# Kernel optimization log

Hardware: AMD Instinct MI355X
Metric: run time of the kernel (lower is better)

## Reference

```python
import jax, jax.numpy as jnp
import numpy as np

N_E = 1024
E_DIM = 64
BETA = 0.25


def setup_inputs() -> dict:
    key = jax.random.key(0)
    k1, k2 = jax.random.split(key)
    z = jax.random.normal(k1, (16, E_DIM, 64, 64), dtype=jnp.float32)
    # embedding initialized uniform(-1/n_e, 1/n_e) as in the torch module
    emb = jax.random.uniform(k2, (N_E, E_DIM), dtype=jnp.float32,
                             minval=-1.0 / N_E, maxval=1.0 / N_E)
    return {"z": z, "emb": emb}


def reference(z, emb):
    n_e, e_dim = emb.shape
    # NCHW -> NHWC, flatten to tokens
    zp = jnp.transpose(z, (0, 2, 3, 1))            # [B,H,W,C]
    zf = zp.reshape(-1, e_dim)                      # [N,C]
    # squared distances ||zf||^2 + ||e||^2 - 2 zf e^T  -> [N, n_e]
    d = (jnp.sum(zf * zf, axis=1, keepdims=True)
         + jnp.sum(emb * emb, axis=1)
         - 2.0 * jnp.matmul(zf, emb.T))
    idx = jnp.argmin(d, axis=1)                     # [N]
    # one-hot @ emb is exactly a gather
    z_q = emb[idx].reshape(zp.shape)                # [B,H,W,C]
    loss = (jnp.mean((jax.lax.stop_gradient(z_q) - zp) ** 2)
            + BETA * jnp.mean((z_q - jax.lax.stop_gradient(zp)) ** 2))
    # straight-through estimator
    z_q = zp + jax.lax.stop_gradient(z_q - zp)
    # perplexity from codeword usage histogram
    counts = jax.ops.segment_sum(jnp.ones_like(idx, dtype=zf.dtype), idx,
                                 num_segments=n_e)
    e_mean = counts / zf.shape[0]
    perplexity = jnp.exp(-jnp.sum(e_mean * jnp.log(e_mean + 1e-10)))
    min_encoding_indices = idx.reshape(z.shape[0], -1).astype(jnp.int32)
    z_q = jnp.transpose(z_q, (0, 3, 1, 2))          # back to NCHW
    return z_q, loss, perplexity, min_encoding_indices
```

## Files before the change

kernel.cpp:

```cpp
#include <hip/hip_runtime.h>

#define TOKS 65536
#define ED 64
#define NE 1024
#define CH_STRIDE 4096
#define B_STRIDE 262144

typedef __bf16 bf16x8 __attribute__((ext_vector_type(8)));
typedef float f32x16 __attribute__((ext_vector_type(16)));
typedef unsigned short ushort_t;
typedef unsigned int uint_t;


__device__ __forceinline__ ushort_t f2bf(float x) {
    uint_t u = __float_as_uint(x);
    uint_t r = u + 0x7FFFu + ((u >> 16) & 1u);
    return (ushort_t)(r >> 16);
}

__global__ __launch_bounds__(256) void vq_prep_e(const float* __restrict__ emb,
                                                 ushort_t* __restrict__ efrag,
                                                 float* __restrict__ enorm,
                                                 int* __restrict__ hist) {
    const int tid = threadIdx.x;
    const int w = tid >> 6, lane = tid & 63;
    const int j = blockIdx.x * 4 + w;

    const float e = emb[j * 64 + lane];
    const float sq = __fmul_rn(e, e);
    float acc = sq;
    acc = __fadd_rn(acc, __shfl_down(sq, 8, 64));
    acc = __fadd_rn(acc, __shfl_down(sq, 16, 64));
    acc = __fadd_rn(acc, __shfl_down(sq, 24, 64));
    acc = __fadd_rn(acc, __shfl_down(sq, 32, 64));
    acc = __fadd_rn(acc, __shfl_down(sq, 40, 64));
    acc = __fadd_rn(acc, __shfl_down(sq, 48, 64));
    acc = __fadd_rn(acc, __shfl_down(sq, 56, 64));
    float x = __fadd_rn(acc, __shfl_down(acc, 1, 64));
    float y = __fadd_rn(x, __shfl_down(x, 2, 64));
    float zn = __fadd_rn(y, __shfl_down(y, 4, 64));
    if (lane == 0) enorm[j] = zn;

    const ushort_t h = f2bf(-2.0f * e);
    const int ct = j >> 5, m = j & 31;
    const int ks = lane >> 4, kh = (lane >> 3) & 1, i = lane & 7;
    efrag[(size_t)((ct * 4 + ks) * 512) + (m + 32 * kh) * 8 + i] = h;

    if (blockIdx.x < 4) hist[blockIdx.x * 256 + tid] = 0;
}

__global__ __launch_bounds__(256, 4) void vq_main(
    const float* __restrict__ z,
    const ushort_t* __restrict__ efrag,
    const float* __restrict__ enorm,
    const float* __restrict__ emb,
    float* __restrict__ zq,
    float* __restrict__ out_idx,
    int* __restrict__ hist,
    double* __restrict__ lossPart) {
    __shared__ float z_s[32][68];
    __shared__ uint_t skey[4][32][2];
    __shared__ unsigned long long s_res[32];
    __shared__ double wsum[4];

    const int tid = threadIdx.x;
    const int w = tid >> 6, lane = tid & 63;
    const int t0 = blockIdx.x * 32;
    const int b = t0 >> 12, hw0 = t0 & 4095;
    const float* zbase = z + (size_t)b * B_STRIDE + hw0;

    {
        const int c = tid >> 2, u0 = (tid & 3) * 8;
        const float* src = zbase + (size_t)c * CH_STRIDE + u0;
        float4 f0 = *(const float4*)(src);
        float4 f1 = *(const float4*)(src + 4);
        z_s[u0 + 0][c] = f0.x; z_s[u0 + 1][c] = f0.y;
        z_s[u0 + 2][c] = f0.z; z_s[u0 + 3][c] = f0.w;
        z_s[u0 + 4][c] = f1.x; z_s[u0 + 5][c] = f1.y;
        z_s[u0 + 6][c] = f1.z; z_s[u0 + 7][c] = f1.w;
    }
    if (tid < 32) s_res[tid] = 0xFFFFFFFFFFFFFFFFull;
    __syncthreads();

    const int n = lane & 31, kh = lane >> 5;

    bf16x8 zb[4];
    #pragma unroll
    for (int ks = 0; ks < 4; ++ks) {
        float4 a0 = *(const float4*)&z_s[n][ks * 16 + kh * 8];
        float4 a1 = *(const float4*)&z_s[n][ks * 16 + kh * 8 + 4];
        const float av[8] = {a0.x, a0.y, a0.z, a0.w, a1.x, a1.y, a1.z, a1.w};
        #pragma unroll
        for (int i = 0; i < 8; ++i) {
            union { ushort_t u; __bf16 bh; } cv;
            cv.u = f2bf(av[i]);
            zb[ks][i] = cv.bh;
        }
    }

    uint_t k0 = 0xFFFFFFFFu, k1 = 0xFFFFFFFFu;
    const bf16x8* eg = (const bf16x8*)efrag;
    const int rot = blockIdx.x & 7;

    int gct = w * 8 + rot;
    bf16x8 ah0 = eg[(size_t)(gct * 4 + 0) * 64 + lane];
    bf16x8 ah1 = eg[(size_t)(gct * 4 + 1) * 64 + lane];
    bf16x8 ah2 = eg[(size_t)(gct * 4 + 2) * 64 + lane];
    bf16x8 ah3 = eg[(size_t)(gct * 4 + 3) * 64 + lane];

    for (int ct = 0; ct < 8; ++ct) {
        const int gnext = w * 8 + ((ct + 1 + rot) & 7);
        bf16x8 nx0, nx1, nx2, nx3;
        if (ct < 7) {
            nx0 = eg[(size_t)(gnext * 4 + 0) * 64 + lane];
            nx1 = eg[(size_t)(gnext * 4 + 1) * 64 + lane];
            nx2 = eg[(size_t)(gnext * 4 + 2) * 64 + lane];
            nx3 = eg[(size_t)(gnext * 4 + 3) * 64 + lane];
        }
        const int jb = gct * 32 + 4 * kh;

        f32x16 acc;
        #pragma unroll
        for (int r = 0; r < 16; ++r) acc[r] = 0.25f;
        acc = __builtin_amdgcn_mfma_f32_32x32x16_bf16(ah0, zb[0], acc, 0, 0, 0);
        acc = __builtin_amdgcn_mfma_f32_32x32x16_bf16(ah1, zb[1], acc, 0, 0, 0);
        acc = __builtin_amdgcn_mfma_f32_32x32x16_bf16(ah2, zb[2], acc, 0, 0, 0);
        acc = __builtin_amdgcn_mfma_f32_32x32x16_bf16(ah3, zb[3], acc, 0, 0, 0);

        #pragma unroll
        for (int r = 0; r < 16; ++r) {
            uint_t key = (__float_as_uint(acc[r]) & 0xFFFFFC00u)
                         | (uint_t)(jb + (r & 3) + 8 * (r >> 2));
            uint_t mx = max(k0, key);
            k1 = min(k1, mx);
            k0 = min(k0, key);
        }
        ah0 = nx0; ah1 = nx1; ah2 = nx2; ah3 = nx3;
        gct = gnext;
    }

    {
        uint_t p0 = (uint_t)__shfl_xor((int)k0, 32, 64);
        uint_t p1 = (uint_t)__shfl_xor((int)k1, 32, 64);
        uint_t o0 = min(k0, p0);
        uint_t o1 = min(max(k0, p0), min(k1, p1));
        if (kh == 0) { skey[w][n][0] = o0; skey[w][n][1] = o1; }
    }
    __syncthreads();

    const int tok = tid >> 3, p = tid & 7;
    const uint_t ck = skey[p >> 1][tok][p & 1];
    uint_t kmin = ck;
    kmin = min(kmin, (uint_t)__shfl_xor((int)kmin, 1, 64));
    kmin = min(kmin, (uint_t)__shfl_xor((int)kmin, 2, 64));
    kmin = min(kmin, (uint_t)__shfl_xor((int)kmin, 4, 64));
    const float thr = __uint_as_float(kmin & 0xFFFFFC00u) + 4.0e-4f;

    float zn;
    {
        float a = z_s[tok][p];
        float racc = __fmul_rn(a, a);
        #pragma unroll
        for (int i = 1; i < 8; ++i) {
            float av = z_s[tok][p + 8 * i];
            racc = __fadd_rn(racc, __fmul_rn(av, av));
        }
        float x1 = __fadd_rn(racc, __shfl_xor(racc, 1, 64));
        float y1 = __fadd_rn(x1, __shfl_xor(x1, 2, 64));
        zn = __fadd_rn(y1, __shfl_xor(y1, 4, 64));
    }

    if (__uint_as_float(ck & 0xFFFFFC00u) <= thr) {
        const int j = (int)(ck & 1023u);
        const float* e = emb + (size_t)j * 64;
        float a0 = 0.f;
        #pragma unroll
        for (int k4 = 0; k4 < 16; ++k4) {
            float4 z4 = *(const float4*)&z_s[tok][k4 * 4];
            float4 e4 = *(const float4*)(e + k4 * 4);
            a0 = __fmaf_rn(z4.x, e4.x, a0);
            a0 = __fmaf_rn(z4.y, e4.y, a0);
            a0 = __fmaf_rn(z4.z, e4.z, a0);
            a0 = __fmaf_rn(z4.w, e4.w, a0);
        }
        float d = __fsub_rn(__fadd_rn(zn, enorm[j]), 2.0f * a0);
        unsigned long long key =
            ((unsigned long long)__float_as_uint(d) << 10)
            | (unsigned long long)j;
        atomicMin(&s_res[tok], key);
    }
    __syncthreads();

    const int bj = (int)(s_res[tok] & 1023u);
    if (p == 0) {
        out_idx[t0 + tok] = (float)bj;
        atomicAdd(&hist[bj], 1);
    }
    double ls = 0.0;
    {
        const float* e = emb + (size_t)bj * 64 + p * 8;
        float4 e0 = *(const float4*)(e);
        float4 e1 = *(const float4*)(e + 4);
        float4 zv0 = *(const float4*)&z_s[tok][p * 8];
        float4 zv1 = *(const float4*)&z_s[tok][p * 8 + 4];
        float df;
        df = e0.x - zv0.x; ls += (double)(df * df);
        df = e0.y - zv0.y; ls += (double)(df * df);
        df = e0.z - zv0.z; ls += (double)(df * df);
        df = e0.w - zv0.w; ls += (double)(df * df);
        df = e1.x - zv1.x; ls += (double)(df * df);
        df = e1.y - zv1.y; ls += (double)(df * df);
        df = e1.z - zv1.z; ls += (double)(df * df);
        df = e1.w - zv1.w; ls += (double)(df * df);
        *(float4*)&z_s[tok][p * 8] = e0;
        *(float4*)&z_s[tok][p * 8 + 4] = e1;
    }
    #pragma unroll
    for (int off = 32; off > 0; off >>= 1) ls += __shfl_down(ls, off, 64);
    if (lane == 0) wsum[w] = ls;
    __syncthreads();
    if (tid == 0)
        lossPart[blockIdx.x] = wsum[0] + wsum[1] + wsum[2] + wsum[3];

    {
        const int c = tid >> 2, u0 = (tid & 3) * 8;
        float4 f0, f1;
        f0.x = z_s[u0 + 0][c]; f0.y = z_s[u0 + 1][c];
        f0.z = z_s[u0 + 2][c]; f0.w = z_s[u0 + 3][c];
        f1.x = z_s[u0 + 4][c]; f1.y = z_s[u0 + 5][c];
        f1.z = z_s[u0 + 6][c]; f1.w = z_s[u0 + 7][c];
        float* dst = zq + (size_t)b * B_STRIDE + (size_t)c * CH_STRIDE + hw0 + u0;
        *(float4*)(dst) = f0;
        *(float4*)(dst + 4) = f1;
    }
}

__global__ __launch_bounds__(256) void vq_final(const int* __restrict__ hist,
                                                const double* __restrict__ lossPart,
                                                float* __restrict__ outs) {
    __shared__ double red[256];
    __shared__ double red2[256];
    double acc = 0.0;
    for (int j = threadIdx.x; j < NE; j += 256) {
        double em = (double)hist[j] * (1.0 / 65536.0);
        acc += em * log(em + 1e-10);
    }
    double lsum = 0.0;
    for (int j = threadIdx.x; j < 2048; j += 256) lsum += lossPart[j];
    red[threadIdx.x] = acc;
    red2[threadIdx.x] = lsum;
    __syncthreads();
    for (int s = 128; s > 0; s >>= 1) {
        if (threadIdx.x < s) {
            red[threadIdx.x] += red[threadIdx.x + s];
            red2[threadIdx.x] += red2[threadIdx.x + s];
        }
        __syncthreads();
    }
    if (threadIdx.x == 0) {
        outs[0] = (float)(1.25 * red2[0] * (1.0 / 4194304.0));
        outs[1] = (float)exp(-red[0]);
    }
}

extern "C" void kernel_launch(void* const* d_in, const int* in_sizes, int n_in,
                              void* d_out, int out_size, void* d_ws, size_t ws_size,
                              hipStream_t stream) {
    const float* z = (const float*)d_in[0];
    const float* emb = (const float*)d_in[1];
    float* out = (float*)d_out;

    char* ws = (char*)d_ws;
    ushort_t* efrag = (ushort_t*)ws;
    float* enorm = (float*)(ws + 131072);
    int* hist = (int*)(ws + 135168);
    double* lossPart = (double*)(ws + 143360);

    float* zq = out;
    float* scalars = out + 4194304;
    float* out_idx = out + 4194306;

    vq_prep_e<<<256, 256, 0, stream>>>(emb, efrag, enorm, hist);
    vq_main<<<2048, 256, 0, stream>>>(z, efrag, enorm, emb, zq, out_idx,
                                      hist, lossPart);
    vq_final<<<1, 256, 0, stream>>>(hist, lossPart, scalars);
}
```

Baseline: 45.26 us.

## Replace top-2 key tracking with min-threshold pass and selective MFMA recompute

The first pass over codebook tiles now keeps only a per-tile float minimum instead of packing index bits into keys and tracking the top two. A second pass recomputes the bf16 MFMA only for tiles whose minimum falls within a threshold of the global minimum, and rescores every candidate within that threshold in exact fp32. This removes the per-element key packing and top-2 logic and makes candidate selection more robust. The cost is repeated efrag loads and MFMAs for qualifying tiles, divergent fp32 dot products, and the loss of the rotation-based prefetch pipelining.

```diff
diff --git a/kernel.cpp b/kernel.cpp
--- a/kernel.cpp
+++ b/kernel.cpp
@@ -59,7 +59,8 @@
     int* __restrict__ hist,
     double* __restrict__ lossPart) {
     __shared__ float z_s[32][68];
-    __shared__ uint_t skey[4][32][2];
+    __shared__ float sminf[4][32];
+    __shared__ float s_zn[32];
     __shared__ unsigned long long s_res[32];
     __shared__ double wsum[4];
 
@@ -98,27 +99,16 @@
         }
     }
 
-    uint_t k0 = 0xFFFFFFFFu, k1 = 0xFFFFFFFFu;
     const bf16x8* eg = (const bf16x8*)efrag;
-    const int rot = blockIdx.x & 7;
-
-    int gct = w * 8 + rot;
-    bf16x8 ah0 = eg[(size_t)(gct * 4 + 0) * 64 + lane];
-    bf16x8 ah1 = eg[(size_t)(gct * 4 + 1) * 64 + lane];
-    bf16x8 ah2 = eg[(size_t)(gct * 4 + 2) * 64 + lane];
-    bf16x8 ah3 = eg[(size_t)(gct * 4 + 3) * 64 + lane];
-
+
+    float mct[8];
+    #pragma unroll
     for (int ct = 0; ct < 8; ++ct) {
-        const int gnext = w * 8 + ((ct + 1 + rot) & 7);
-        bf16x8 nx0, nx1, nx2, nx3;
-        if (ct < 7) {
-            nx0 = eg[(size_t)(gnext * 4 + 0) * 64 + lane];
-            nx1 = eg[(size_t)(gnext * 4 + 1) * 64 + lane];
-            nx2 = eg[(size_t)(gnext * 4 + 2) * 64 + lane];
-            nx3 = eg[(size_t)(gnext * 4 + 3) * 64 + lane];
-        }
-        const int jb = gct * 32 + 4 * kh;
-
+        const int gct = w * 8 + ct;
+        bf16x8 ah0 = eg[(size_t)(gct * 4 + 0) * 64 + lane];
+        bf16x8 ah1 = eg[(size_t)(gct * 4 + 1) * 64 + lane];
+        bf16x8 ah2 = eg[(size_t)(gct * 4 + 2) * 64 + lane];
+        bf16x8 ah3 = eg[(size_t)(gct * 4 + 3) * 64 + lane];
         f32x16 acc;
         #pragma unroll
         for (int r = 0; r < 16; ++r) acc[r] = 0.25f;
@@ -126,38 +116,23 @@
         acc = __builtin_amdgcn_mfma_f32_32x32x16_bf16(ah1, zb[1], acc, 0, 0, 0);
         acc = __builtin_amdgcn_mfma_f32_32x32x16_bf16(ah2, zb[2], acc, 0, 0, 0);
         acc = __builtin_amdgcn_mfma_f32_32x32x16_bf16(ah3, zb[3], acc, 0, 0, 0);
-
-        #pragma unroll
-        for (int r = 0; r < 16; ++r) {
-            uint_t key = (__float_as_uint(acc[r]) & 0xFFFFFC00u)
-                         | (uint_t)(jb + (r & 3) + 8 * (r >> 2));
-            uint_t mx = max(k0, key);
-            k1 = min(k1, mx);
-            k0 = min(k0, key);
-        }
-        ah0 = nx0; ah1 = nx1; ah2 = nx2; ah3 = nx3;
-        gct = gnext;
-    }
-
-    {
-        uint_t p0 = (uint_t)__shfl_xor((int)k0, 32, 64);
-        uint_t p1 = (uint_t)__shfl_xor((int)k1, 32, 64);
-        uint_t o0 = min(k0, p0);
-        uint_t o1 = min(max(k0, p0), min(k1, p1));
-        if (kh == 0) { skey[w][n][0] = o0; skey[w][n][1] = o1; }
-    }
-    __syncthreads();
-
-    const int tok = tid >> 3, p = tid & 7;
-    const uint_t ck = skey[p >> 1][tok][p & 1];
-    uint_t kmin = ck;
-    kmin = min(kmin, (uint_t)__shfl_xor((int)kmin, 1, 64));
-    kmin = min(kmin, (uint_t)__shfl_xor((int)kmin, 2, 64));
-    kmin = min(kmin, (uint_t)__shfl_xor((int)kmin, 4, 64));
-    const float thr = __uint_as_float(kmin & 0xFFFFFC00u) + 4.0e-4f;
-
-    float zn;
-    {
+        float m0 = fminf(fminf(acc[0], acc[1]), fminf(acc[2], acc[3]));
+        float m1 = fminf(fminf(acc[4], acc[5]), fminf(acc[6], acc[7]));
+        float m2 = fminf(fminf(acc[8], acc[9]), fminf(acc[10], acc[11]));
+        float m3 = fminf(fminf(acc[12], acc[13]), fminf(acc[14], acc[15]));
+        mct[ct] = fminf(fminf(m0, m1), fminf(m2, m3));
+    }
+    {
+        float vmin = mct[0];
+        #pragma unroll
+        for (int ct = 1; ct < 8; ++ct) vmin = fminf(vmin, mct[ct]);
+        vmin = fminf(vmin, __shfl_xor(vmin, 32, 64));
+        if (kh == 0) sminf[w][n] = vmin;
+    }
+    __syncthreads();
+
+    {
+        const int tok = tid >> 3, p = tid & 7;
         float a = z_s[tok][p];
         float racc = __fmul_rn(a, a);
         #pragma unroll
@@ -167,30 +142,56 @@
         }
         float x1 = __fadd_rn(racc, __shfl_xor(racc, 1, 64));
         float y1 = __fadd_rn(x1, __shfl_xor(x1, 2, 64));
-        zn = __fadd_rn(y1, __shfl_xor(y1, 4, 64));
-    }
-
-    if (__uint_as_float(ck & 0xFFFFFC00u) <= thr) {
-        const int j = (int)(ck & 1023u);
-        const float* e = emb + (size_t)j * 64;
-        float a0 = 0.f;
-        #pragma unroll
-        for (int k4 = 0; k4 < 16; ++k4) {
-            float4 z4 = *(const float4*)&z_s[tok][k4 * 4];
-            float4 e4 = *(const float4*)(e + k4 * 4);
-            a0 = __fmaf_rn(z4.x, e4.x, a0);
-            a0 = __fmaf_rn(z4.y, e4.y, a0);
-            a0 = __fmaf_rn(z4.z, e4.z, a0);
-            a0 = __fmaf_rn(z4.w, e4.w, a0);
-        }
-        float d = __fsub_rn(__fadd_rn(zn, enorm[j]), 2.0f * a0);
-        unsigned long long key =
-            ((unsigned long long)__float_as_uint(d) << 10)
-            | (unsigned long long)j;
-        atomicMin(&s_res[tok], key);
-    }
-    __syncthreads();
-
+        float znv = __fadd_rn(y1, __shfl_xor(y1, 4, 64));
+        if (p == 0) s_zn[tok] = znv;
+    }
+    __syncthreads();
+
+    const float thr = fminf(fminf(sminf[0][n], sminf[1][n]),
+                            fminf(sminf[2][n], sminf[3][n])) + 4.0e-4f;
+    const float zn = s_zn[n];
+    #pragma unroll 1
+    for (int ct = 0; ct < 8; ++ct) {
+        if (__any(mct[ct] <= thr)) {
+            const int gct = w * 8 + ct;
+            bf16x8 ah0 = eg[(size_t)(gct * 4 + 0) * 64 + lane];
+            bf16x8 ah1 = eg[(size_t)(gct * 4 + 1) * 64 + lane];
+            bf16x8 ah2 = eg[(size_t)(gct * 4 + 2) * 64 + lane];
+            bf16x8 ah3 = eg[(size_t)(gct * 4 + 3) * 64 + lane];
+            f32x16 acc;
+            #pragma unroll
+            for (int r = 0; r < 16; ++r) acc[r] = 0.25f;
+            acc = __builtin_amdgcn_mfma_f32_32x32x16_bf16(ah0, zb[0], acc, 0, 0, 0);
+            acc = __builtin_amdgcn_mfma_f32_32x32x16_bf16(ah1, zb[1], acc, 0, 0, 0);
+            acc = __builtin_amdgcn_mfma_f32_32x32x16_bf16(ah2, zb[2], acc, 0, 0, 0);
+            acc = __builtin_amdgcn_mfma_f32_32x32x16_bf16(ah3, zb[3], acc, 0, 0, 0);
+            #pragma unroll
+            for (int r = 0; r < 16; ++r) {
+                if (acc[r] <= thr) {
+                    const int j = gct * 32 + (r & 3) + 8 * (r >> 2) + 4 * kh;
+                    const float* e = emb + (size_t)j * 64;
+                    float a0 = 0.f;
+                    #pragma unroll
+                    for (int k4 = 0; k4 < 16; ++k4) {
+                        float4 z4 = *(const float4*)&z_s[n][k4 * 4];
+                        float4 e4 = *(const float4*)(e + k4 * 4);
+                        a0 = __fmaf_rn(z4.x, e4.x, a0);
+                        a0 = __fmaf_rn(z4.y, e4.y, a0);
+                        a0 = __fmaf_rn(z4.z, e4.z, a0);
+                        a0 = __fmaf_rn(z4.w, e4.w, a0);
+                    }
+                    float d = __fsub_rn(__fadd_rn(zn, enorm[j]), 2.0f * a0);
+                    unsigned long long key =
+                        ((unsigned long long)__float_as_uint(d) << 10)
+                        | (unsigned long long)j;
+                    atomicMin(&s_res[n], key);
+                }
+            }
+        }
+    }
+    __syncthreads();
+
+    const int tok = tid >> 3, p = tid & 7;
     const int bj = (int)(s_res[tok] & 1023u);
     if (p == 0) {
         out_idx[t0 + tok] = (float)bj;
```

Result: slower. 82.82 us (+83.0%).
